# Kernel optimization log

Measured on AMD Instinct MI355X. Metric: run time of the kernel, lower is better.

Reference implementation:

```python
import jax, jax.numpy as jnp
import numpy as np

B, T, I, H = 64, 2048, 256, 256


def setup_inputs() -> dict:
    key = jax.random.key(0)
    ks = jax.random.split(key, 6)
    s = 1.0 / np.sqrt(H)
    x = jax.random.normal(ks[0], (B, T, I), dtype=jnp.float32)
    att_weights = jax.random.uniform(ks[1], (B, T), dtype=jnp.float32)
    lengths = jax.random.randint(ks[2], (B,), 1, T + 1, dtype=jnp.int32)
    W_ih = jax.random.uniform(ks[3], (3 * H, I), minval=-s, maxval=s, dtype=jnp.float32)
    W_hh = jax.random.uniform(ks[4], (3 * H, H), minval=-s, maxval=s, dtype=jnp.float32)
    b_ih = jax.random.uniform(ks[5], (3 * H,), minval=-s, maxval=s, dtype=jnp.float32)
    b_hh = jax.random.uniform(jax.random.fold_in(key, 7), (3 * H,), minval=-s, maxval=s, dtype=jnp.float32)
    return {"x": x, "att_weights": att_weights, "lengths": lengths,
            "W_ih": W_ih, "W_hh": W_hh, "b_ih": b_ih, "b_hh": b_hh}


def reference(x, att_weights, lengths, W_ih, W_hh, b_ih, b_hh):
    # x: [B, T, I]; att_weights: [B, T]; lengths: [B]
    Bv, Tv, _ = x.shape
    Hv = W_hh.shape[1]
    # Padded equivalent of the packed-sequence loop: update h only while t < length.
    mask = jnp.arange(Tv)[None, :] < lengths[:, None]  # [B, T]

    def step(h, inp):
        xt, wt, mt = inp  # [B, I], [B], [B]
        gi = xt @ W_ih.T + b_ih  # [B, 3H]
        gh = h @ W_hh.T + b_hh   # [B, 3H]
        i_r, i_z, i_n = jnp.split(gi, 3, axis=-1)
        h_r, h_z, h_n = jnp.split(gh, 3, axis=-1)
        r = jax.nn.sigmoid(i_r + h_r)
        z = jax.nn.sigmoid(i_z + h_z)
        n = jnp.tanh(i_n + r * h_n)
        h_new = (1.0 - z) * n + z * h  # GRUCell output
        w = wt[:, None]
        h_gated = w * h_new + (1.0 - w) * h  # attention gating
        h = jnp.where(mt[:, None], h_gated, h)
        return h, None

    h0 = jnp.zeros((Bv, Hv), dtype=x.dtype)
    xs = (jnp.swapaxes(x, 0, 1), att_weights.T, mask.T)  # time-major
    hT, _ = jax.lax.scan(step, h0, xs)
    return hT  # [B, H]
```

## Files before the change

kernel.cpp:

```cpp
#include <hip/hip_runtime.h>
#include <stdint.h>

#define B_ 64
#define T_ 2048
#define I_ 256
#define H_ 256
#define G3 768
#define NPROD 192
#define CH 16
#define NTILE_N 6

typedef _Float16 half2v __attribute__((ext_vector_type(2)));
typedef _Float16 half8v __attribute__((ext_vector_type(8)));

#if __has_builtin(__builtin_amdgcn_fdot2)
#define FDOT2(a, b, c) __builtin_amdgcn_fdot2((a), (b), (c), false)
#else
#define FDOT2(a, b, c) fmaf((float)(a)[1], (float)(b)[1], fmaf((float)(a)[0], (float)(b)[0], (c)))
#endif

__global__ void zero_flags(int* __restrict__ done, int n)
{
  int i = threadIdx.x + blockIdx.x * blockDim.x;
  if (i < n) __hip_atomic_store(&done[i], 0, __ATOMIC_RELAXED, __HIP_MEMORY_SCOPE_AGENT);
}

__global__ __launch_bounds__(512) __attribute__((amdgpu_waves_per_eu(2, 2)))
void fused(const float* __restrict__ x, const float* __restrict__ att,
           const int* __restrict__ lengths, const float* __restrict__ Wih,
           const float* __restrict__ Whh, const float* __restrict__ bih,
           const float* __restrict__ bhh, float* __restrict__ gi,
           int* __restrict__ done, float* __restrict__ hws,
           float* __restrict__ out, int t0, int t1)
{
  __shared__ __align__(16) float smem[32 * 68 + 32 * 132];
  const int tid = threadIdx.x;
  const int Tc = t1 - t0;

  if (blockIdx.x >= B_) {
    const int pid = blockIdx.x - B_;
    float* As = smem;
    float* Bs = smem + 32 * 68;
    const int ty = tid >> 5, tx = tid & 31;
    const int lr = tid >> 3;
    const int lk = (tid & 7) << 2;
    const int NT = Tc * NTILE_N;
    for (int i = pid; i < NT; i += NPROD) {
      const int rel = i / NTILE_N;
      const int tt  = t0 + rel;
      const int n0  = (i % NTILE_N) << 7;
      float acc[4][4] = {};
      for (int kc = 0; kc < I_; kc += 32) {
        float4 a0 = *(const float4*)(x + ((size_t)lr * T_ + tt) * I_ + kc + lk);
        float4 b0 = *(const float4*)(Wih + (size_t)(n0 + lr) * I_ + kc + lk);
        float4 b1 = *(const float4*)(Wih + (size_t)(n0 + lr + 64) * I_ + kc + lk);
        __syncthreads();
        As[(lk + 0) * 68 + lr] = a0.x; As[(lk + 1) * 68 + lr] = a0.y;
        As[(lk + 2) * 68 + lr] = a0.z; As[(lk + 3) * 68 + lr] = a0.w;
        Bs[(lk + 0) * 132 + lr] = b0.x; Bs[(lk + 1) * 132 + lr] = b0.y;
        Bs[(lk + 2) * 132 + lr] = b0.z; Bs[(lk + 3) * 132 + lr] = b0.w;
        Bs[(lk + 0) * 132 + lr + 64] = b1.x; Bs[(lk + 1) * 132 + lr + 64] = b1.y;
        Bs[(lk + 2) * 132 + lr + 64] = b1.z; Bs[(lk + 3) * 132 + lr + 64] = b1.w;
        __syncthreads();
        #pragma unroll
        for (int kk = 0; kk < 32; ++kk) {
          float4 av = *(const float4*)(&As[kk * 68 + (ty << 2)]);
          float4 bv = *(const float4*)(&Bs[kk * 132 + (tx << 2)]);
          float av_[4] = {av.x, av.y, av.z, av.w};
          float bv_[4] = {bv.x, bv.y, bv.z, bv.w};
          #pragma unroll
          for (int u = 0; u < 4; ++u)
            #pragma unroll
            for (int v = 0; v < 4; ++v)
              acc[u][v] = fmaf(av_[u], bv_[v], acc[u][v]);
        }
      }
      const int colb = n0 + (tx << 2);
      float4 bi = *(const float4*)(bih + colb);
      float4 bh = *(const float4*)(bhh + colb);
      float4 badd;
      badd.x = bi.x + (colb + 0 < 512 ? bh.x : 0.f);
      badd.y = bi.y + (colb + 1 < 512 ? bh.y : 0.f);
      badd.z = bi.z + (colb + 2 < 512 ? bh.z : 0.f);
      badd.w = bi.w + (colb + 3 < 512 ? bh.w : 0.f);
      float* gout = gi + (size_t)rel * B_ * G3;
      #pragma unroll
      for (int r = 0; r < 4; ++r) {
        const int bb = (ty << 2) + r;
        float4 o;
        o.x = acc[r][0] + badd.x; o.y = acc[r][1] + badd.y;
        o.z = acc[r][2] + badd.z; o.w = acc[r][3] + badd.w;
        *(float4*)(gout + (size_t)bb * G3 + colb) = o;
      }
      __syncthreads();
      if (tid == 0) {
        __threadfence();
        __hip_atomic_fetch_add(&done[rel >> 4], 1, __ATOMIC_RELEASE, __HIP_MEMORY_SCOPE_AGENT);
      }
    }
    return;
  }

  const int b  = blockIdx.x;
  const int j  = tid >> 1;
  const int s  = tid & 1;
  const int k0 = s << 7;
  _Float16* hbuf  = (_Float16*)smem;
  float*    att_s = smem + 384;

  half2v w[192];
  #pragma unroll
  for (int g = 0; g < 3; ++g) {
    const float* row = Whh + (size_t)(g * 256 + j) * H_ + k0;
    #pragma unroll
    for (int q = 0; q < 32; ++q) {
      float4 v = *(const float4*)(row + (q << 2));
      half2v a, c;
      a[0] = (_Float16)v.x; a[1] = (_Float16)v.y;
      c[0] = (_Float16)v.z; c[1] = (_Float16)v.w;
      w[g * 64 + 2 * q]     = a;
      w[g * 64 + 2 * q + 1] = c;
    }
  }

  float bhn = 0.f, h_reg = 0.f;
  if (s == 0) {
    bhn = bhh[512 + j];
    h_reg = (t0 > 0) ? hws[b * H_ + j] : 0.f;
  }
  if (tid < 256) {
    float v = (t0 > 0) ? hws[b * H_ + tid] : 0.f;
    hbuf[(tid >> 7) * 136 + (tid & 127)] = (_Float16)v;
  }
  for (int i = tid; i < Tc; i += 512) att_s[i] = att[(size_t)b * T_ + t0 + i];
  int len = lengths[b]; if (len > t1) len = t1;
  const int nch = (Tc + CH - 1) / CH;
  int wm = -1;
  __syncthreads();

#define GATE(NEED) do {                                                               \
    int need_ = (NEED); if (need_ > nch - 1) need_ = nch - 1;                         \
    if (need_ > wm) {                                                                 \
      if (tid == 0) {                                                                 \
        for (int c_ = wm + 1; c_ <= need_; ++c_) {                                    \
          int exp_ = ((Tc - c_ * CH) < CH ? (Tc - c_ * CH) : CH) * NTILE_N;           \
          while (__hip_atomic_load(&done[c_], __ATOMIC_RELAXED,                       \
                                   __HIP_MEMORY_SCOPE_AGENT) < exp_)                  \
            __builtin_amdgcn_s_sleep(2);                                              \
        }                                                                             \
      }                                                                               \
      __syncthreads();                                                                \
      __threadfence();       \
      wm = need_;                                                                     \
    }                                                                                 \
  } while (0)

#define STEP(CGR, CGZ, CGN, NGR, NGZ, NGN, TT, ISSUE_OK) do {                         \
    if (s == 0 && (ISSUE_OK)) {                                                       \
      const float* gb_ = gi + ((size_t)((TT) + 2 - t0) * B_ + b) * G3;                \
      NGR = gb_[j]; NGZ = gb_[256 + j]; NGN = gb_[512 + j];                           \
    }                                                                                 \
    float wat_ = (s == 0) ? att_s[(TT) - t0] : 0.f;                                   \
    float accr = 0.f, accz = 0.f, accn = 0.f;                                         \
    const _Float16* hb = hbuf + p * 272 + s * 136;                                    \
    _Pragma("unroll")                                                                 \
    for (int q = 0; q < 16; ++q) {                                                    \
      half8v hv = *(const half8v*)(hb + (q << 3));                                    \
      half2v h0_ = __builtin_shufflevector(hv, hv, 0, 1);                             \
      half2v h1_ = __builtin_shufflevector(hv, hv, 2, 3);                             \
      half2v h2_ = __builtin_shufflevector(hv, hv, 4, 5);                             \
      half2v h3_ = __builtin_shufflevector(hv, hv, 6, 7);                             \
      const int qq = q << 2;                                                          \
      accr = FDOT2(w[qq + 0], h0_, accr);                                             \
      accr = FDOT2(w[qq + 1], h1_, accr);                                             \
      accr = FDOT2(w[qq + 2], h2_, accr);                                             \
      accr = FDOT2(w[qq + 3], h3_, accr);                                             \
      accz = FDOT2(w[64 + qq + 0], h0_, accz);                                        \
      accz = FDOT2(w[64 + qq + 1], h1_, accz);                                        \
      accz = FDOT2(w[64 + qq + 2], h2_, accz);                                        \
      accz = FDOT2(w[64 + qq + 3], h3_, accz);                                        \
      accn = FDOT2(w[128 + qq + 0], h0_, accn);                                       \
      accn = FDOT2(w[128 + qq + 1], h1_, accn);                                       \
      accn = FDOT2(w[128 + qq + 2], h2_, accn);                                       \
      accn = FDOT2(w[128 + qq + 3], h3_, accn);                                       \
    }                                                                                 \
    accr += __shfl_xor(accr, 1);                                                      \
    accz += __shfl_xor(accz, 1);                                                      \
    accn += __shfl_xor(accn, 1);                                                      \
    if (s == 0) {                                                                     \
      float r_ = 1.f / (1.f + __expf(-(accr + CGR)));                                 \
      float z_ = 1.f / (1.f + __expf(-(accz + CGZ)));                                 \
      float e2_ = __expf(2.f * (CGN + r_ * (accn + bhn)));                            \
      float nn_ = 1.f - 2.f / (e2_ + 1.f);                                            \
      float hnew_ = (1.f - z_) * nn_ + z_ * h_reg;                                    \
      h_reg = wat_ * hnew_ + (1.f - wat_) * h_reg;                                    \
      hbuf[(p ^ 1) * 272 + (j >> 7) * 136 + (j & 127)] = (_Float16)h_reg;             \
    }                                                                                 \
    __syncthreads();                                                                  \
    p ^= 1;                                                                           \
  } while (0)

  GATE(0);
  float e_gr = 0.f, e_gz = 0.f, e_gn = 0.f;
  float o_gr = 0.f, o_gz = 0.f, o_gn = 0.f;
  float e2_gr = 0.f, e2_gz = 0.f, e2_gn = 0.f;
  float o2_gr = 0.f, o2_gz = 0.f, o2_gn = 0.f;
  if (s == 0 && t0 < len) {
    const float* gb = gi + (size_t)b * G3;
    e_gr = gb[j]; e_gz = gb[256 + j]; e_gn = gb[512 + j];
  }
  if (s == 0 && t0 + 1 < len) {
    const float* gb = gi + ((size_t)B_ + b) * G3;
    o_gr = gb[j]; o_gz = gb[256 + j]; o_gn = gb[512 + j];
  }

  int p = 0;
  int t = t0;
  for (; t + 1 < len; t += 2) {
    GATE((t + 3 - t0) >> 4);
    STEP(e_gr, e_gz, e_gn, e2_gr, e2_gz, e2_gn, t,     (t + 2 < len));
    STEP(o_gr, o_gz, o_gn, o2_gr, o2_gz, o2_gn, t + 1, (t + 3 < len));
    e_gr = e2_gr; e_gz = e2_gz; e_gn = e2_gn;
    o_gr = o2_gr; o_gz = o2_gz; o_gn = o2_gn;
  }
  if (t < len) {
    STEP(e_gr, e_gz, e_gn, e2_gr, e2_gz, e2_gn, t, false);
  }

  if (s == 0) {
    hws[b * H_ + j] = h_reg;
    if (t1 == T_) out[b * H_ + j] = h_reg;
  }
#undef STEP
#undef GATE
}

extern "C" void kernel_launch(void* const* d_in, const int* in_sizes, int n_in,
                              void* d_out, int out_size, void* d_ws, size_t ws_size,
                              hipStream_t stream)
{
  const float* x       = (const float*)d_in[0];
  const float* att     = (const float*)d_in[1];
  const int*   lengths = (const int*)d_in[2];
  const float* Wih     = (const float*)d_in[3];
  const float* Whh     = (const float*)d_in[4];
  const float* bih     = (const float*)d_in[5];
  const float* bhh     = (const float*)d_in[6];
  float* out = (float*)d_out;

  int*   done = (int*)d_ws;
  float* hws  = (float*)((char*)d_ws + 4096);
  float* gi   = (float*)((char*)d_ws + 4096 + 65536);
  const size_t used0 = 4096 + 65536;
  const size_t per_t = (size_t)B_ * G3 * sizeof(float);
  size_t avail = ws_size > used0 ? ws_size - used0 : 0;
  int Tc = (int)(avail / per_t);
  if (Tc > T_) Tc = T_;
  if (Tc < 1) Tc = 1;

  for (int t0 = 0; t0 < T_; t0 += Tc) {
    int t1 = t0 + Tc; if (t1 > T_) t1 = T_;
    int nch = (t1 - t0 + CH - 1) / CH;
    zero_flags<<<dim3((nch + 127) / 128), 128, 0, stream>>>(done, nch);
    fused<<<dim3(B_ + NPROD), 512, 0, stream>>>(x, att, lengths, Wih, Whh, bih, bhh,
                                                gi, done, hws, out, t0, t1);
  }
}
```

Before: 3.554 ms.

## Deepen gate-input prefetch to four steps and use LDS-only barrier wait

Reworks the recurrent loop so the precomputed input-gate values are prefetched four timesteps ahead, using four rotating register sets and a 4x unrolled loop. Each global load is now issued after the step's compute instead of before it. The block-wide __syncthreads is replaced by an s_waitcnt that waits only on LDS/scalar counters followed by s_barrier, so the in-flight global loads no longer stall the per-step barrier. This aims to hide global-memory latency on the serial critical path. The cost is more live registers, and correctness now depends on the gate/GATE ordering still covering the deeper prefetch distance.

```diff
diff --git a/kernel.cpp b/kernel.cpp
--- a/kernel.cpp
+++ b/kernel.cpp
@@ -18,6 +18,11 @@
 #else
 #define FDOT2(a, b, c) fmaf((float)(a)[1], (float)(b)[1], fmaf((float)(a)[0], (float)(b)[0], (c)))
 #endif
+
+#define BAR_LGKM() do {                      \
+    __builtin_amdgcn_s_waitcnt(0xC07F);      \
+    __builtin_amdgcn_s_barrier();            \
+  } while (0)
 
 __global__ void zero_flags(int* __restrict__ done, int n)
 {
@@ -155,11 +160,7 @@
     }                                                                                 \
   } while (0)
 
-#define STEP(CGR, CGZ, CGN, NGR, NGZ, NGN, TT, ISSUE_OK) do {                         \
-    if (s == 0 && (ISSUE_OK)) {                                                       \
-      const float* gb_ = gi + ((size_t)((TT) + 2 - t0) * B_ + b) * G3;                \
-      NGR = gb_[j]; NGZ = gb_[256 + j]; NGN = gb_[512 + j];                           \
-    }                                                                                 \
+#define STEP(GR, GZ, GN, TT, ISSUE_OK) do {                                           \
     float wat_ = (s == 0) ? att_s[(TT) - t0] : 0.f;                                   \
     float accr = 0.f, accz = 0.f, accn = 0.f;                                         \
     const _Float16* hb = hbuf + p * 272 + s * 136;                                    \
@@ -188,44 +189,56 @@
     accz += __shfl_xor(accz, 1);                                                      \
     accn += __shfl_xor(accn, 1);                                                      \
     if (s == 0) {                                                                     \
-      float r_ = 1.f / (1.f + __expf(-(accr + CGR)));                                 \
-      float z_ = 1.f / (1.f + __expf(-(accz + CGZ)));                                 \
-      float e2_ = __expf(2.f * (CGN + r_ * (accn + bhn)));                            \
+      float r_ = 1.f / (1.f + __expf(-(accr + GR)));                                  \
+      float z_ = 1.f / (1.f + __expf(-(accz + GZ)));                                  \
+      float e2_ = __expf(2.f * (GN + r_ * (accn + bhn)));                             \
       float nn_ = 1.f - 2.f / (e2_ + 1.f);                                            \
       float hnew_ = (1.f - z_) * nn_ + z_ * h_reg;                                    \
       h_reg = wat_ * hnew_ + (1.f - wat_) * h_reg;                                    \
       hbuf[(p ^ 1) * 272 + (j >> 7) * 136 + (j & 127)] = (_Float16)h_reg;             \
     }                                                                                 \
-    __syncthreads();                                                                  \
+    if (s == 0 && (ISSUE_OK)) {                      \
+      const float* gb_ = gi + ((size_t)((TT) + 4 - t0) * B_ + b) * G3;                \
+      GR = gb_[j]; GZ = gb_[256 + j]; GN = gb_[512 + j];                              \
+    }                                                                                 \
+    BAR_LGKM();                                                                       \
     p ^= 1;                                                                           \
   } while (0)
 
   GATE(0);
-  float e_gr = 0.f, e_gz = 0.f, e_gn = 0.f;
-  float o_gr = 0.f, o_gz = 0.f, o_gn = 0.f;
-  float e2_gr = 0.f, e2_gz = 0.f, e2_gn = 0.f;
-  float o2_gr = 0.f, o2_gz = 0.f, o2_gn = 0.f;
-  if (s == 0 && t0 < len) {
-    const float* gb = gi + (size_t)b * G3;
-    e_gr = gb[j]; e_gz = gb[256 + j]; e_gn = gb[512 + j];
+  float a_gr = 0.f, a_gz = 0.f, a_gn = 0.f;
+  float b_gr = 0.f, b_gz = 0.f, b_gn = 0.f;
+  float c_gr = 0.f, c_gz = 0.f, c_gn = 0.f;
+  float d_gr = 0.f, d_gz = 0.f, d_gn = 0.f;
+  if (s == 0 && t0 + 0 < len) {
+    const float* gb = gi + ((size_t)0 * B_ + b) * G3;
+    a_gr = gb[j]; a_gz = gb[256 + j]; a_gn = gb[512 + j];
   }
   if (s == 0 && t0 + 1 < len) {
-    const float* gb = gi + ((size_t)B_ + b) * G3;
-    o_gr = gb[j]; o_gz = gb[256 + j]; o_gn = gb[512 + j];
+    const float* gb = gi + ((size_t)1 * B_ + b) * G3;
+    b_gr = gb[j]; b_gz = gb[256 + j]; b_gn = gb[512 + j];
+  }
+  if (s == 0 && t0 + 2 < len) {
+    const float* gb = gi + ((size_t)2 * B_ + b) * G3;
+    c_gr = gb[j]; c_gz = gb[256 + j]; c_gn = gb[512 + j];
+  }
+  if (s == 0 && t0 + 3 < len) {
+    const float* gb = gi + ((size_t)3 * B_ + b) * G3;
+    d_gr = gb[j]; d_gz = gb[256 + j]; d_gn = gb[512 + j];
   }
 
   int p = 0;
   int t = t0;
-  for (; t + 1 < len; t += 2) {
-    GATE((t + 3 - t0) >> 4);
-    STEP(e_gr, e_gz, e_gn, e2_gr, e2_gz, e2_gn, t,     (t + 2 < len));
-    STEP(o_gr, o_gz, o_gn, o2_gr, o2_gz, o2_gn, t + 1, (t + 3 < len));
-    e_gr = e2_gr; e_gz = e2_gz; e_gn = e2_gn;
-    o_gr = o2_gr; o_gz = o2_gz; o_gn = o2_gn;
-  }
-  if (t < len) {
-    STEP(e_gr, e_gz, e_gn, e2_gr, e2_gz, e2_gn, t, false);
-  }
+  for (; t + 3 < len; t += 4) {
+    GATE((t + 7 - t0) >> 4);
+    STEP(a_gr, a_gz, a_gn, t,     (t + 4 < len));
+    STEP(b_gr, b_gz, b_gn, t + 1, (t + 5 < len));
+    STEP(c_gr, c_gz, c_gn, t + 2, (t + 6 < len));
+    STEP(d_gr, d_gz, d_gn, t + 3, (t + 7 < len));
+  }
+  if (t < len) { STEP(a_gr, a_gz, a_gn, t, false); ++t; }
+  if (t < len) { STEP(b_gr, b_gz, b_gn, t, false); ++t; }
+  if (t < len) { STEP(c_gr, c_gz, c_gn, t, false); ++t; }
 
   if (s == 0) {
     hws[b * H_ + j] = h_reg;
```

New measurement: 3.710 ms. +4.4%, slower.
